# Optimization experiments

Measured on AMD Instinct MI355X. Metric: run time of the kernel, lower is better.

## Reference

```python
import jax, jax.numpy as jnp
import numpy as np

BLOCK_SIZE = 64
HIDDEN = 1024
INTERMEDIATE = 4096
NUM_BLOCK = HIDDEN // BLOCK_SIZE              # 16
INT_BLOCK = (INTERMEDIATE // HIDDEN) * BLOCK_SIZE  # 256


def setup_inputs() -> dict:
    key = jax.random.key(0)
    k_x, k_w1, k_b1, k_w2, k_b2 = jax.random.split(key, 5)
    hidden_states = jax.random.normal(k_x, (4, 2048, HIDDEN), dtype=jnp.float32)
    w1 = 0.02 * jax.random.normal(k_w1, (NUM_BLOCK, INT_BLOCK, BLOCK_SIZE), dtype=jnp.float32)
    b1 = 0.001 * jax.random.normal(k_b1, (INTERMEDIATE,), dtype=jnp.float32)
    w2 = 0.02 * jax.random.normal(k_w2, (NUM_BLOCK, BLOCK_SIZE, INT_BLOCK), dtype=jnp.float32)
    b2 = 0.001 * jax.random.normal(k_b2, (HIDDEN,), dtype=jnp.float32)
    return {"hidden_states": hidden_states, "w1": w1, "b1": b1, "w2": w2, "b2": b2}


def reference(hidden_states, w1, b1, w2, b2):
    lead = hidden_states.shape[:-1]
    dim = hidden_states.shape[-1]
    nb, ibs, bs = w1.shape  # num_block, intermediate_block_size, block_size
    x = hidden_states.reshape(-1, nb, bs)                 # [B, n, i]
    h = jnp.einsum('bni,noi->bno', x, w1)                 # [B, n, o]
    # channel shuffle: transpose block and feature axes before flattening
    h = jnp.swapaxes(h, -1, -2).reshape(-1, nb * ibs)     # [B, o*n order]
    h = jax.nn.gelu(h + b1, approximate=False)
    h = h.reshape(-1, nb, ibs)                            # regroup after shuffle
    y = jnp.einsum('bni,noi->bno', h, w2).reshape(-1, nb * bs) + b2
    return y.reshape(*lead, dim)
```

## Files before the change

### kernel.cpp

```cpp
#include <hip/hip_runtime.h>
#include <hip/hip_bf16.h>


typedef __attribute__((ext_vector_type(8))) short  short8;
typedef __attribute__((ext_vector_type(4))) short  short4v;
typedef __attribute__((ext_vector_type(4))) float  floatx4;

#define XPITCH 72

__device__ __forceinline__ short f2bf(float f) {
  union { __hip_bfloat16 h; short s; } u;
  u.h = __float2bfloat16(f);
  return u.s;
}
__device__ __forceinline__ float bf2f(short s) {
  union { float f; unsigned u; } uu;
  uu.u = ((unsigned)(unsigned short)s) << 16;
  return uu.f;
}

__device__ __forceinline__ float gelu_f(float v) {
  float m = v * v;
  float c = fmaf(-0.1029375f, m, -2.3020807f);
  float z = v * c;
  float e = __builtin_amdgcn_exp2f(z);
  return v * __builtin_amdgcn_rcpf(1.0f + e);
}

__global__ void pack_k(const float* __restrict__ w1, const float* __restrict__ w2,
                       const float* __restrict__ b1, short* __restrict__ w1p,
                       short* __restrict__ w2p, short* __restrict__ b1p) {
  const int t = blockIdx.x * blockDim.x + threadIdx.x;
  const int lane = t & 63;
  const int lhi = lane >> 4;
  if (t < 32768) {
    const int ks = (t >> 6) & 1, np = (t >> 7) & 15, n = (t >> 11) & 15;
    const float* src = w1 + ((size_t)(n * 256 + np * 16 + (lane & 15)) * 64 + ks * 32 + lhi * 8);
    short8 f;
#pragma unroll
    for (int e = 0; e < 8; ++e) f[e] = f2bf(src[e]);
    *(short8*)(w1p + (size_t)t * 8) = f;
  } else if (t < 65536) {
    const int t2 = t - 32768;
    const int ot = (t2 >> 6) & 3, ks = (t2 >> 8) & 7, np = (t2 >> 11) & 15;
    const int op = ot * 16 + (lane & 15);
    short8 f;
#pragma unroll
    for (int e = 0; e < 8; ++e) {
      const int k = ks * 32 + lhi * 8 + e;
      f[e] = f2bf(w2[(size_t)(np * 64 + op) * 256 + (k & 15) * 16 + (k >> 4)]);
    }
    *(short8*)(w2p + (size_t)t2 * 8) = f;
  } else {
    const int t3 = t - 65536;
    const int np = (t3 >> 6) & 15, n = (t3 >> 10) & 15;
    short4v b;
#pragma unroll
    for (int r = 0; r < 4; ++r) b[r] = f2bf(b1[(np * 16 + lhi * 4 + r) * 16 + n]);
    *(short4v*)(b1p + (size_t)((n * 16 + np) * 64 + lane) * 4) = b;
  }
}

__global__ __launch_bounds__(256, 4) void k1_gemm1(
    const float* __restrict__ x, const short* __restrict__ w1p,
    const short* __restrict__ b1p, short* __restrict__ G) {
  __shared__ __align__(16) short xs[128 * XPITCH];

  const int tid = threadIdx.x;
  const int wv = tid >> 6, lane = tid & 63;
  const int l15 = lane & 15, lhi = lane >> 4;
  const int b   = blockIdx.x;
  const int n   = b >> 6;
  const int rtg = b & 63;
  const int np0 = wv * 4;

  short8  wf[4][2];
  short4v bv[4];
#pragma unroll
  for (int j = 0; j < 4; ++j) {
    const int np = np0 + j;
    wf[j][0] = *(const short8*)(w1p + (size_t)(((n * 16 + np) * 2 + 0) * 64 + lane) * 8);
    wf[j][1] = *(const short8*)(w1p + (size_t)(((n * 16 + np) * 2 + 1) * 64 + lane) * 8);
    bv[j]    = *(const short4v*)(b1p + (size_t)((n * 16 + np) * 64 + lane) * 4);
  }

  {
    const int rr = tid >> 4;
    const int cc = (tid & 15) * 4;
    const float* px = x + (size_t)(rtg * 128 + rr) * 1024 + n * 64 + cc;
#pragma unroll
    for (int p = 0; p < 8; ++p) {
      floatx4 v = *(const floatx4*)(px + (size_t)p * 16 * 1024);
      short4v s;
#pragma unroll
      for (int e = 0; e < 4; ++e) s[e] = f2bf(v[e]);
      *(short4v*)(&xs[(p * 16 + rr) * XPITCH + cc]) = s;
    }
  }
  __syncthreads();

#pragma unroll
  for (int rt = 0; rt < 8; ++rt) {
    const short* xrow = &xs[(rt * 16 + l15) * XPITCH];
    short8 xf0 = *(const short8*)(xrow + lhi * 8);
    short8 xf1 = *(const short8*)(xrow + 32 + lhi * 8);
    short* gb = G + (size_t)(rtg * 8 + rt) * 65536 + n * 256 + l15 * 16 + lhi * 4;
#pragma unroll
    for (int j = 0; j < 4; ++j) {
      floatx4 acc = {0.f, 0.f, 0.f, 0.f};
      acc = __builtin_amdgcn_mfma_f32_16x16x32_bf16(wf[j][0], xf0, acc, 0, 0, 0);
      acc = __builtin_amdgcn_mfma_f32_16x16x32_bf16(wf[j][1], xf1, acc, 0, 0, 0);
      short4v hv;
#pragma unroll
      for (int e = 0; e < 4; ++e)
        hv[e] = f2bf(gelu_f(acc[e] + bf2f(bv[j][e])));
      *(short4v*)(gb + (size_t)(np0 + j) * 4096) = hv;
    }
  }
}

__global__ __launch_bounds__(256, 4) void k2_gemm2(
    const short* __restrict__ G, const short* __restrict__ w2p,
    const float* __restrict__ b2, float* __restrict__ y) {
  const int tid = threadIdx.x;
  const int wv = tid >> 6, lane = tid & 63;
  const int l15 = lane & 15, lhi = lane >> 4;
  const int rt = blockIdx.x >> 2;
  const int np = (blockIdx.x & 3) * 4 + wv;

  const short* ab = G + (size_t)(rt * 16 + np) * 4096 + (lhi >> 1) * 256 + l15 * 16 + (lhi & 1) * 8;
  short8 af[8];
#pragma unroll
  for (int ks = 0; ks < 8; ++ks)
    af[ks] = *(const short8*)(ab + ks * 512);

#pragma unroll
  for (int ot = 0; ot < 4; ++ot) {
    floatx4 a0 = {0.f, 0.f, 0.f, 0.f}, a1 = {0.f, 0.f, 0.f, 0.f};
#pragma unroll
    for (int ks = 0; ks < 8; ks += 2) {
      short8 b0  = *(const short8*)(w2p + (size_t)(((np * 8 + ks) * 4 + ot) * 64 + lane) * 8);
      short8 b1f = *(const short8*)(w2p + (size_t)(((np * 8 + ks + 1) * 4 + ot) * 64 + lane) * 8);
      a0 = __builtin_amdgcn_mfma_f32_16x16x32_bf16(af[ks], b0, a0, 0, 0, 0);
      a1 = __builtin_amdgcn_mfma_f32_16x16x32_bf16(af[ks + 1], b1f, a1, 0, 0, 0);
    }
    const int col = np * 64 + ot * 16 + l15;
    const float bb = b2[col];
    float* py = y + (size_t)(rt * 16 + lhi * 4) * 1024 + col;
#pragma unroll
    for (int r = 0; r < 4; ++r)
      py[(size_t)r * 1024] = a0[r] + a1[r] + bb;
  }
}

extern "C" void kernel_launch(void* const* d_in, const int* in_sizes, int n_in,
                              void* d_out, int out_size, void* d_ws, size_t ws_size,
                              hipStream_t stream) {
  const float* x  = (const float*)d_in[0];
  const float* w1 = (const float*)d_in[1];
  const float* b1 = (const float*)d_in[2];
  const float* w2 = (const float*)d_in[3];
  const float* b2 = (const float*)d_in[4];
  float* y = (float*)d_out;

  short* w1p = (short*)d_ws;
  short* w2p = w1p + 16 * 256 * 64;
  short* b1p = w2p + 16 * 256 * 64;
  short* G   = b1p + 16 * 16 * 64 * 4;

  pack_k<<<160, 512, 0, stream>>>(w1, w2, b1, w1p, w2p, b1p);
  k1_gemm1<<<1024, 256, 0, stream>>>(x, w1p, b1p, G);
  k2_gemm2<<<2048, 256, 0, stream>>>(G, w2p, b2, y);
}
```

Baseline: 49.36 us.

## Fuse both block-diagonal GEMMs into one kernel, keeping intermediate in LDS

Replaces the two-kernel pipeline (GEMM1+GELU writing a bf16 intermediate to global memory, then GEMM2 reading it back) with a single fused kernel. Each block loads a 16-row tile of x into swizzled shared memory, computes GEMM1 chunks per output group, stages the GELU results in a per-wave LDS buffer and feeds them straight into GEMM2 accumulators. This removes the 64 MB-scale intermediate round trip and a kernel launch. In exchange, weights are reloaded from global/L2 per block instead of held in registers, and the x tile is read by two blocks.

```diff
diff --git a/kernel.cpp b/kernel.cpp
--- a/kernel.cpp
+++ b/kernel.cpp
@@ -5,8 +5,6 @@
 typedef __attribute__((ext_vector_type(8))) short  short8;
 typedef __attribute__((ext_vector_type(4))) short  short4v;
 typedef __attribute__((ext_vector_type(4))) float  floatx4;
-
-#define XPITCH 72
 
 __device__ __forceinline__ short f2bf(float f) {
   union { __hip_bfloat16 h; short s; } u;
@@ -61,95 +59,83 @@
   }
 }
 
-__global__ __launch_bounds__(256, 4) void k1_gemm1(
+__global__ __launch_bounds__(256, 4) void fused_k(
     const float* __restrict__ x, const short* __restrict__ w1p,
-    const short* __restrict__ b1p, short* __restrict__ G) {
-  __shared__ __align__(16) short xs[128 * XPITCH];
+    const short* __restrict__ w2p, const short* __restrict__ b1p,
+    const float* __restrict__ b2, float* __restrict__ y) {
+  __shared__ __align__(16) short xs[16 * 1024];
+  __shared__ __align__(16) short ch[4 * 16 * 64];
 
   const int tid = threadIdx.x;
   const int wv = tid >> 6, lane = tid & 63;
   const int l15 = lane & 15, lhi = lane >> 4;
-  const int b   = blockIdx.x;
-  const int n   = b >> 6;
-  const int rtg = b & 63;
-  const int np0 = wv * 4;
+  const int rt  = blockIdx.x >> 1;
+  const int nph = blockIdx.x & 1;
 
-  short8  wf[4][2];
-  short4v bv[4];
 #pragma unroll
-  for (int j = 0; j < 4; ++j) {
-    const int np = np0 + j;
-    wf[j][0] = *(const short8*)(w1p + (size_t)(((n * 16 + np) * 2 + 0) * 64 + lane) * 8);
-    wf[j][1] = *(const short8*)(w1p + (size_t)(((n * 16 + np) * 2 + 1) * 64 + lane) * 8);
-    bv[j]    = *(const short4v*)(b1p + (size_t)((n * 16 + np) * 64 + lane) * 4);
-  }
-
-  {
-    const int rr = tid >> 4;
-    const int cc = (tid & 15) * 4;
-    const float* px = x + (size_t)(rtg * 128 + rr) * 1024 + n * 64 + cc;
+  for (int p = 0; p < 4; ++p) {
+    const int row = wv * 4 + p;
+    const int rsw = (row & 7) << 3;
 #pragma unroll
-    for (int p = 0; p < 8; ++p) {
-      floatx4 v = *(const floatx4*)(px + (size_t)p * 16 * 1024);
+    for (int q = 0; q < 4; ++q) {
+      const int col = q * 256 + lane * 4;
+      floatx4 v = *(const floatx4*)(x + (size_t)(rt * 16 + row) * 1024 + col);
       short4v s;
 #pragma unroll
       for (int e = 0; e < 4; ++e) s[e] = f2bf(v[e]);
-      *(short4v*)(&xs[(p * 16 + rr) * XPITCH + cc]) = s;
+      *(short4v*)(&xs[row * 1024 + (col ^ rsw)]) = s;
     }
   }
   __syncthreads();
 
-#pragma unroll
-  for (int rt = 0; rt < 8; ++rt) {
-    const short* xrow = &xs[(rt * 16 + l15) * XPITCH];
-    short8 xf0 = *(const short8*)(xrow + lhi * 8);
-    short8 xf1 = *(const short8*)(xrow + 32 + lhi * 8);
-    short* gb = G + (size_t)(rtg * 8 + rt) * 65536 + n * 256 + l15 * 16 + lhi * 4;
-#pragma unroll
-    for (int j = 0; j < 4; ++j) {
-      floatx4 acc = {0.f, 0.f, 0.f, 0.f};
-      acc = __builtin_amdgcn_mfma_f32_16x16x32_bf16(wf[j][0], xf0, acc, 0, 0, 0);
-      acc = __builtin_amdgcn_mfma_f32_16x16x32_bf16(wf[j][1], xf1, acc, 0, 0, 0);
-      short4v hv;
-#pragma unroll
-      for (int e = 0; e < 4; ++e)
-        hv[e] = f2bf(gelu_f(acc[e] + bf2f(bv[j][e])));
-      *(short4v*)(gb + (size_t)(np0 + j) * 4096) = hv;
-    }
-  }
-}
-
-__global__ __launch_bounds__(256, 4) void k2_gemm2(
-    const short* __restrict__ G, const short* __restrict__ w2p,
-    const float* __restrict__ b2, float* __restrict__ y) {
-  const int tid = threadIdx.x;
-  const int wv = tid >> 6, lane = tid & 63;
-  const int l15 = lane & 15, lhi = lane >> 4;
-  const int rt = blockIdx.x >> 2;
-  const int np = (blockIdx.x & 3) * 4 + wv;
-
-  const short* ab = G + (size_t)(rt * 16 + np) * 4096 + (lhi >> 1) * 256 + l15 * 16 + (lhi & 1) * 8;
-  short8 af[8];
-#pragma unroll
-  for (int ks = 0; ks < 8; ++ks)
-    af[ks] = *(const short8*)(ab + ks * 512);
+  const int swz = (l15 & 7) << 3;
+  short* myc = ch + wv * 1024;
 
 #pragma unroll
-  for (int ot = 0; ot < 4; ++ot) {
-    floatx4 a0 = {0.f, 0.f, 0.f, 0.f}, a1 = {0.f, 0.f, 0.f, 0.f};
+  for (int it = 0; it < 2; ++it) {
+    const int np = nph * 8 + wv * 2 + it;
+    floatx4 acc2[4] = {{0.f,0.f,0.f,0.f},{0.f,0.f,0.f,0.f},
+                       {0.f,0.f,0.f,0.f},{0.f,0.f,0.f,0.f}};
+
 #pragma unroll
-    for (int ks = 0; ks < 8; ks += 2) {
-      short8 b0  = *(const short8*)(w2p + (size_t)(((np * 8 + ks) * 4 + ot) * 64 + lane) * 8);
-      short8 b1f = *(const short8*)(w2p + (size_t)(((np * 8 + ks + 1) * 4 + ot) * 64 + lane) * 8);
-      a0 = __builtin_amdgcn_mfma_f32_16x16x32_bf16(af[ks], b0, a0, 0, 0, 0);
-      a1 = __builtin_amdgcn_mfma_f32_16x16x32_bf16(af[ks + 1], b1f, a1, 0, 0, 0);
+    for (int h = 0; h < 4; ++h) {
+#pragma unroll
+      for (int nn = 0; nn < 4; ++nn) {
+        const int n = h * 4 + nn;
+        short8 xf0 = *(const short8*)(&xs[l15 * 1024 + ((n * 64 + lhi * 8) ^ swz)]);
+        short8 xf1 = *(const short8*)(&xs[l15 * 1024 + ((n * 64 + 32 + lhi * 8) ^ swz)]);
+        short8 wf0 = *(const short8*)(w1p + (size_t)(((n * 16 + np) * 2 + 0) * 64 + lane) * 8);
+        short8 wf1 = *(const short8*)(w1p + (size_t)(((n * 16 + np) * 2 + 1) * 64 + lane) * 8);
+        short4v bv = *(const short4v*)(b1p + (size_t)((n * 16 + np) * 64 + lane) * 4);
+        floatx4 acc = {0.f, 0.f, 0.f, 0.f};
+        acc = __builtin_amdgcn_mfma_f32_16x16x32_bf16(wf0, xf0, acc, 0, 0, 0);
+        acc = __builtin_amdgcn_mfma_f32_16x16x32_bf16(wf1, xf1, acc, 0, 0, 0);
+        short4v hv;
+#pragma unroll
+        for (int e = 0; e < 4; ++e)
+          hv[e] = f2bf(gelu_f(acc[e] + bf2f(bv[e])));
+        *(short4v*)(&myc[l15 * 64 + ((nn * 16 + lhi * 4) ^ swz)]) = hv;
+      }
+      short8 af0 = *(const short8*)(&myc[l15 * 64 + ((0 * 32 + lhi * 8) ^ swz)]);
+      short8 af1 = *(const short8*)(&myc[l15 * 64 + ((1 * 32 + lhi * 8) ^ swz)]);
+#pragma unroll
+      for (int ot = 0; ot < 4; ++ot) {
+        short8 bf0 = *(const short8*)(w2p + (size_t)(((np * 8 + 2 * h) * 4 + ot) * 64 + lane) * 8);
+        short8 bf1 = *(const short8*)(w2p + (size_t)(((np * 8 + 2 * h + 1) * 4 + ot) * 64 + lane) * 8);
+        acc2[ot] = __builtin_amdgcn_mfma_f32_16x16x32_bf16(af0, bf0, acc2[ot], 0, 0, 0);
+        acc2[ot] = __builtin_amdgcn_mfma_f32_16x16x32_bf16(af1, bf1, acc2[ot], 0, 0, 0);
+      }
     }
-    const int col = np * 64 + ot * 16 + l15;
-    const float bb = b2[col];
-    float* py = y + (size_t)(rt * 16 + lhi * 4) * 1024 + col;
+
 #pragma unroll
-    for (int r = 0; r < 4; ++r)
-      py[(size_t)r * 1024] = a0[r] + a1[r] + bb;
+    for (int ot = 0; ot < 4; ++ot) {
+      const int col = np * 64 + ot * 16 + l15;
+      const float bb = b2[col];
+      float* py = y + (size_t)(rt * 16 + lhi * 4) * 1024 + col;
+#pragma unroll
+      for (int r = 0; r < 4; ++r)
+        py[(size_t)r * 1024] = acc2[ot][r] + bb;
+    }
   }
 }
 
@@ -166,9 +152,7 @@
   short* w1p = (short*)d_ws;
   short* w2p = w1p + 16 * 256 * 64;
   short* b1p = w2p + 16 * 256 * 64;
-  short* G   = b1p + 16 * 16 * 64 * 4;
 
   pack_k<<<160, 512, 0, stream>>>(w1, w2, b1, w1p, w2p, b1p);
-  k1_gemm1<<<1024, 256, 0, stream>>>(x, w1p, b1p, G);
-  k2_gemm2<<<2048, 256, 0, stream>>>(G, w2p, b2, y);
+  fused_k<<<1024, 256, 0, stream>>>(x, w1p, w2p, b1p, b2, y);
 }
```

New measurement: 48.28 us. 1.02x faster.
